# Kernel optimization log

Measured on AMD Instinct MI355X. Metric: run time of the kernel, lower is better.

The kernel has to match this reference:

```python
import jax, jax.numpy as jnp
import numpy as np
from jax.scipy.special import logsumexp

TAG_NAMES = ['<pad>', 'O', 'B-PER', 'I-PER', 'B-LOC', 'I-LOC', 'B-ORG', 'I-ORG', 'B-MISC', 'I-MISC']
K = len(TAG_NAMES)
T, B, D = 512, 64, 1024
PAD = 0
IMP = -100.0
VOCAB = 30000


def _crf_params(rng):
    # torchcrf reset_parameters: uniform(-0.1, 0.1), then init_crf_transitions overrides
    start = rng.uniform(-0.1, 0.1, K).astype(np.float32)
    end = rng.uniform(-0.1, 0.1, K).astype(np.float32)
    trans = rng.uniform(-0.1, 0.1, (K, K)).astype(np.float32)
    for i, name in enumerate(TAG_NAMES):
        if name[0] in ('I', 'L') or name == '<pad>':
            start[i] = IMP
        if name[0] in ('B', 'I'):
            end[i] = IMP
    tag_is = {p: [i for i, t in enumerate(TAG_NAMES) if t[0] == p] for p in 'BIOUL'}
    tag_is['P'] = [i for i, t in enumerate(TAG_NAMES) if t == 'tag']
    for ft, tos in {'B': 'BOUP', 'I': 'BOUP', 'O': 'IL', 'U': 'IL'}.items():
        for fi in tag_is[ft]:
            for tt in tos:
                for ti in tag_is[tt]:
                    trans[fi, ti] = IMP
    for ft, tos in {'B': 'IL', 'I': 'IL'}.items():
        for fi in tag_is[ft]:
            for tt in tos:
                for ti in tag_is[tt]:
                    if TAG_NAMES[fi].split('-')[1] != TAG_NAMES[ti].split('-')[1]:
                        trans[fi, ti] = IMP
    return jnp.asarray(start), jnp.asarray(end), jnp.asarray(trans)


def setup_inputs() -> dict:
    rng = np.random.default_rng(0)
    # torchcrf requires mask[0] == 1 everywhere and contiguous masks -> build from lengths
    lengths = rng.integers(T // 2, T + 1, size=B)
    valid = np.arange(T)[:, None] < lengths[None, :]  # (T, B)
    words = np.where(valid, rng.integers(1, VOCAB, size=(T, B)), PAD).astype(np.int64)
    tags = rng.integers(0, K, size=(T, B)).astype(np.int64)
    word_features = rng.standard_normal((T, B, D)).astype(np.float32)
    W = (rng.standard_normal((D, K)) / np.sqrt(D)).astype(np.float32)
    b = np.zeros(K, np.float32)
    start, end, trans = _crf_params(rng)
    return dict(words=jnp.asarray(words), tags=jnp.asarray(tags),
                word_features=jnp.asarray(word_features), W=jnp.asarray(W), b=jnp.asarray(b),
                start_trans=start, end_trans=end, transitions=trans)


def _crf_loss(emissions, tags, maskf, start, end, trans):
    """-log p(tags | emissions), summed over batch (torchcrf reduction='sum')."""
    bidx = jnp.arange(emissions.shape[1])
    # gold-path score (numerator)
    score0 = start[tags[0]] + emissions[0, bidx, tags[0]]
    em_tag = jnp.take_along_axis(emissions[1:], tags[1:, :, None], axis=-1)[..., 0]  # (T-1,B)
    step = trans[tags[:-1], tags[1:]] + em_tag
    numer = score0 + jnp.sum(step * maskf[1:], axis=0)
    seq_ends = maskf.sum(0).astype(jnp.int32) - 1
    numer = numer + end[tags[seq_ends, bidx]]
    # partition function (forward algorithm, stable log-sum-exp scan)
    def fwd_step(score, xs):
        em_t, m_t = xs
        nxt = logsumexp(score[:, :, None] + trans[None] + em_t[:, None, :], axis=1)  # (B,K)
        return jnp.where(m_t[:, None] > 0, nxt, score), None
    score, _ = jax.lax.scan(fwd_step, start[None] + emissions[0], (emissions[1:], maskf[1:]))
    denom = logsumexp(score + end[None], axis=1)
    return -(numer - denom).sum()


def _crf_decode(emissions, maskf, start, end, trans):
    """Viterbi decode; returns (T,B) int32 paths, 0-padded past sequence ends."""
    bidx = jnp.arange(emissions.shape[1])
    def vit_step(score, xs):
        em_t, m_t = xs
        bcast = score[:, :, None] + trans[None] + em_t[:, None, :]  # (B, K_prev, K_cur)
        best = bcast.max(axis=1)
        idx = bcast.argmax(axis=1).astype(jnp.int32)
        return jnp.where(m_t[:, None] > 0, best, score), idx
    score, history = jax.lax.scan(vit_step, start[None] + emissions[0], (emissions[1:], maskf[1:]))
    last_tag = jnp.argmax(score + end[None], axis=1).astype(jnp.int32)  # tag at seq_end per batch
    def back_step(tag, xs):
        hist_t, m_t = xs
        prev = jnp.where(m_t > 0, hist_t[bidx, tag], tag)
        return prev, prev
    _, path_head = jax.lax.scan(back_step, last_tag, (history, maskf[1:]), reverse=True)
    paths = jnp.concatenate([path_head, last_tag[None]], axis=0)  # (T, B)
    return jnp.where(maskf > 0, paths, 0)


def reference(words, tags, word_features, W, b, start_trans, end_trans, transitions):
    # eval-mode dropout is identity; fc projects features to tag emissions
    emissions = word_features @ W + b  # (T, B, K)
    maskf = (words != PAD).astype(emissions.dtype)  # (T, B)
    paths = _crf_decode(emissions, maskf, start_trans, end_trans, transitions)
    loss = _crf_loss(emissions, tags, maskf, start_trans, end_trans, transitions)
    return paths, loss
```

## Files before the change

kernel.cpp:

```cpp
#include <hip/hip_runtime.h>
#include <hip/hip_bf16.h>

#define TT 512
#define BB 64
#define KK 10
#define DD 1024
#define CL 32
#define NC 16

typedef unsigned char uchar;
typedef short bf16x8 __attribute__((ext_vector_type(8)));
typedef float f32x4 __attribute__((ext_vector_type(4)));

__device__ __forceinline__ unsigned f2bf(float f) {
    unsigned u = __float_as_uint(f);
    return (u + 0x7FFFu + ((u >> 16) & 1u)) >> 16;
}

__device__ __forceinline__ float max10(const float* r) {
    float m0 = fmaxf(r[0], r[1]), m1 = fmaxf(r[2], r[3]);
    float m2 = fmaxf(r[4], r[5]), m3 = fmaxf(r[6], r[7]);
    float m4 = fmaxf(r[8], r[9]);
    m0 = fmaxf(m0, m1); m2 = fmaxf(m2, m3); m0 = fmaxf(m0, m2);
    return fmaxf(m0, m4);
}

__device__ __forceinline__ float lse10(const float* r) {
    const float m = max10(r);
    float s0 = __expf(r[0] - m) + __expf(r[1] - m);
    float s1 = __expf(r[2] - m) + __expf(r[3] - m);
    float s2 = __expf(r[4] - m) + __expf(r[5] - m);
    float s3 = __expf(r[6] - m) + __expf(r[7] - m);
    float s4 = __expf(r[8] - m) + __expf(r[9] - m);
    return m + __logf(((s0 + s1) + (s2 + s3)) + s4);
}

__global__ __launch_bounds__(512) void k_emissions(
    const int* __restrict__ words, const float* __restrict__ wf,
    const float* __restrict__ W, const float* __restrict__ bias,
    float* __restrict__ em, int* __restrict__ lenArr, float* loss_slot) {
    __shared__ char  Ab[2][128 * 256];
    __shared__ uint4 Bfrag[32][64];
    __shared__ int   cnt[8][64];

    const int tid = threadIdx.x;

    for (int idx = tid; idx < 32 * 64; idx += 512) {
        const int ks = idx >> 6, l = idx & 63;
        const int col = l & 15, kg = l >> 4;
        unsigned u[4];
        #pragma unroll
        for (int p = 0; p < 4; ++p) {
            unsigned lo = 0, hi = 0;
            if (col < KK) {
                const int k0 = ks * 32 + kg * 8 + p * 2;
                lo = f2bf(W[(size_t)k0 * KK + col]);
                hi = f2bf(W[(size_t)(k0 + 1) * KK + col]);
            }
            u[p] = lo | (hi << 16);
        }
        Bfrag[ks][l] = make_uint4(u[0], u[1], u[2], u[3]);
    }

    const int wave = tid >> 6, lane = tid & 63;
    const int arow = lane & 15;
    const int kg   = lane >> 4;
    const int row0blk = blockIdx.x * 128;

    const int srow = tid >> 5;
    const int scol = (tid & 31) * 4;
    const float* gbase = wf + (size_t)(row0blk + srow) * DD + scol;
    const int wr_off = srow * 256 + (((scol >> 3) ^ srow) << 4) + ((scol & 7) * 2);

    float4 st[8];
    #pragma unroll
    for (int i = 0; i < 8; ++i) st[i] = *(const float4*)(gbase + i * 16384);
    #pragma unroll
    for (int i = 0; i < 8; ++i) {
        uint2 w;
        w.x = (__float_as_uint(st[i].x) >> 16) | (__float_as_uint(st[i].y) & 0xFFFF0000u);
        w.y = (__float_as_uint(st[i].z) >> 16) | (__float_as_uint(st[i].w) & 0xFFFF0000u);
        *(uint2*)(&Ab[0][wr_off + i * 4096]) = w;
    }
    #pragma unroll
    for (int i = 0; i < 8; ++i) st[i] = *(const float4*)(gbase + 128 + i * 16384);
    __syncthreads();

    f32x4 acc = {0.f, 0.f, 0.f, 0.f};
    const int ldsrow = wave * 16 + arow;

    #pragma unroll 1
    for (int p = 0; p < 8; ++p) {
        if (p < 7) {
            if (p > 0) __syncthreads();
            char* wb = Ab[(p + 1) & 1];
            #pragma unroll
            for (int i = 0; i < 8; ++i) {
                uint2 w;
                w.x = (__float_as_uint(st[i].x) >> 16) | (__float_as_uint(st[i].y) & 0xFFFF0000u);
                w.y = (__float_as_uint(st[i].z) >> 16) | (__float_as_uint(st[i].w) & 0xFFFF0000u);
                *(uint2*)(&wb[wr_off + i * 4096]) = w;
            }
            if (p < 6) {
                const float* gp = gbase + (size_t)(p + 2) * 128;
                #pragma unroll
                for (int i = 0; i < 8; ++i) st[i] = *(const float4*)(gp + i * 16384);
            }
            __syncthreads();
        }
        const char* rb = &Ab[p & 1][ldsrow * 256];
        #pragma unroll
        for (int ks = 0; ks < 4; ++ks) {
            const bf16x8 a = *(const bf16x8*)(rb + (((ks * 4 + kg) ^ arow) << 4));
            union { uint4 u; bf16x8 v; } bu;
            bu.u = Bfrag[p * 4 + ks][lane];
            acc = __builtin_amdgcn_mfma_f32_16x16x32_bf16(a, bu.v, acc, 0, 0, 0);
        }
    }

    const int row0 = row0blk + wave * 16;
    if (arow < KK) {
        const float bk = bias[arow];
        #pragma unroll
        for (int r = 0; r < 4; ++r)
            em[(size_t)(row0 + kg * 4 + r) * KK + arow] = acc[r] + bk;
    }

    if (blockIdx.x == 0) {
        const int b = tid & 63, seg = tid >> 6;
        int c = 0;
        for (int t = seg; t < TT; t += 8) c += (words[t * BB + b] != 0) ? 1 : 0;
        cnt[seg][b] = c;
        __syncthreads();
        if (tid < 64) {
            int s = 0;
            #pragma unroll
            for (int g = 0; g < 8; ++g) s += cnt[g][tid];
            lenArr[tid] = s;
        }
        if (tid == 0) *loss_slot = 0.f;
    }
}

__global__ __launch_bounds__(128) void k_chunk(
    const float* __restrict__ em, const float* __restrict__ trans,
    const int* __restrict__ lenArr, float* __restrict__ Mlse, float* __restrict__ Mmax) {
    int id = blockIdx.x;
    const bool mx = id >= 1024; id &= 1023;
    const int b = id >> 4, c = id & 15;
    const int len = lenArr[b];
    const int s_lo = c * CL + 1;
    const int s_hi = min(c * CL + CL, len - 1);
    const int ns = s_hi - s_lo + 1;
    if (ns <= 0) return;

    __shared__ float Ms[KK][12];
    __shared__ float eml[CL][KK];
    const int tid = threadIdx.x;
    for (int idx = tid; idx < CL * KK; idx += 128) {
        const int sl = idx / KK, j = idx % KK;
        const int s = s_lo + sl;
        eml[sl][j] = (s <= TT - 1) ? em[((size_t)s * BB + b) * KK + j] : 0.f;
    }
    const int i = tid / KK, j = tid % KK;
    const bool act = tid < KK * KK;
    float trc[KK];
    if (act) {
        #pragma unroll
        for (int k = 0; k < KK; ++k) trc[k] = trans[k * KK + j];
    }
    __syncthreads();
    float cur = 0.f;
    if (act) { cur = trans[i * KK + j] + eml[0][j]; Ms[i][j] = cur; }
    __syncthreads();
    for (int sl = 1; sl < ns; ++sl) {
        float row[KK];
        if (act) {
            #pragma unroll
            for (int k = 0; k < KK; ++k) row[k] = Ms[i][k] + trc[k];
        }
        __syncthreads();
        if (act) {
            cur = (mx ? max10(row) : lse10(row)) + eml[sl][j];
            Ms[i][j] = cur;
        }
        __syncthreads();
    }
    if (act) {
        float* out = mx ? Mmax : Mlse;
        out[((size_t)b * NC + c) * 100 + i * KK + j] = cur;
    }
}

__global__ __launch_bounds__(1024) void k_crf(
    const int* __restrict__ tags, const float* __restrict__ em,
    const float* __restrict__ startv, const float* __restrict__ endv,
    const float* __restrict__ trans, const int* __restrict__ lenArr,
    const float* __restrict__ Mlse, const float* __restrict__ Mmax,
    int* __restrict__ paths, float* __restrict__ loss_slot) {
    const int b = blockIdx.x;
    const int tid = threadIdx.x;
    const int wv = tid >> 6, lane = tid & 63;
    const int len = lenArr[b];

    __shared__ float Ml[NC][100];
    __shared__ float Mm[NC][100];
    __shared__ float eml[NC][CL][KK];
    __shared__ float ub[NC][KK];
    __shared__ uchar hl[NC][CL * KK];
    __shared__ int   Fl[NC][KK];
    __shared__ int   vt[NC + 1];
    __shared__ float em0[KK];
    __shared__ float red[2];

    for (int idx = tid; idx < NC * 100; idx += 1024) {
        Ml[idx / 100][idx % 100] = Mlse[(size_t)b * NC * 100 + idx];
        Mm[idx / 100][idx % 100] = Mmax[(size_t)b * NC * 100 + idx];
    }
    for (int idx = tid; idx < NC * CL * KK; idx += 1024) {
        const int c = idx / (CL * KK), r = idx % (CL * KK);
        const int sl = r / KK, j = r % KK;
        const int s = c * CL + 1 + sl;
        eml[c][sl][j] = (s <= TT - 1) ? em[((size_t)s * BB + b) * KK + j] : 0.f;
    }
    if (tid < KK) em0[tid] = em[(size_t)b * KK + tid];
    __syncthreads();

    if (wv == 0) {
        float v[KK];
        #pragma unroll
        for (int i = 0; i < KK; ++i) v[i] = startv[i] + em0[i];
        for (int c = 0; c < NC; ++c) {
            if (lane < KK) ub[c][lane] = v[lane];
            const int s_hi = min(c * CL + CL, len - 1);
            if (s_hi >= c * CL + 1) {
                float nv = 0.f;
                if (lane < KK) {
                    float r[KK];
                    #pragma unroll
                    for (int k = 0; k < KK; ++k) r[k] = v[k] + Mm[c][k * KK + lane];
                    nv = max10(r);
                }
                #pragma unroll
                for (int i = 0; i < KK; ++i) v[i] = __shfl(nv, i);
            }
        }
        float best = v[0] + endv[0];
        int bi = 0;
        #pragma unroll
        for (int i = 1; i < KK; ++i) {
            const float x = v[i] + endv[i];
            if (x > best) { best = x; bi = i; }
        }
        if (lane == 0) vt[NC] = bi;
    } else if (wv == 1) {
        float v[KK];
        #pragma unroll
        for (int i = 0; i < KK; ++i) v[i] = startv[i] + em0[i];
        for (int c = 0; c < NC; ++c) {
            const int s_hi = min(c * CL + CL, len - 1);
            if (s_hi >= c * CL + 1) {
                float nv = 0.f;
                if (lane < KK) {
                    float r[KK];
                    #pragma unroll
                    for (int k = 0; k < KK; ++k) r[k] = v[k] + Ml[c][k * KK + lane];
                    nv = lse10(r);
                }
                #pragma unroll
                for (int i = 0; i < KK; ++i) v[i] = __shfl(nv, i);
            }
        }
        float r[KK];
        #pragma unroll
        for (int i = 0; i < KK; ++i) r[i] = v[i] + endv[i];
        if (lane == 0) red[0] = lse10(r);
    } else if (wv == 2) {
        float part = 0.f;
        for (int t = 1 + lane; t < len; t += 64) {
            const int tp = tags[(t - 1) * BB + b];
            const int tc = tags[t * BB + b];
            part += trans[tp * KK + tc] + eml[(t - 1) >> 5][(t - 1) & 31][tc];
        }
        #pragma unroll
        for (int off = 32; off >= 1; off >>= 1) part += __shfl_xor(part, off);
        if (lane == 0) {
            const int t0 = tags[b];
            const int te = tags[(len - 1) * BB + b];
            red[1] = part + startv[t0] + em0[t0] + endv[te];
        }
    }
    __syncthreads();

    {
        const int c = wv;
        const int s_hi = min(c * CL + CL, len - 1);
        const int ns = s_hi - (c * CL + 1) + 1;
        if (ns > 0) {
            float trc[KK];
            if (lane < KK) {
                #pragma unroll
                for (int i = 0; i < KK; ++i) trc[i] = trans[i * KK + lane];
            }
            float s[KK];
            #pragma unroll
            for (int i = 0; i < KK; ++i) s[i] = ub[c][i];
            for (int sl = 0; sl < ns; ++sl) {
                float best = s[0] + trc[0];
                int bi = 0;
                #pragma unroll
                for (int i = 1; i < KK; ++i) {
                    const float x = s[i] + trc[i];
                    if (x > best) { best = x; bi = i; }
                }
                float snew = 0.f;
                if (lane < KK) {
                    snew = best + eml[c][sl][lane];
                    hl[c][sl * KK + lane] = (uchar)bi;
                }
                #pragma unroll
                for (int i = 0; i < KK; ++i) s[i] = __shfl(snew, i);
            }
            if (lane < KK) {
                int cur = lane;
                for (int sl = ns - 1; sl >= 0; --sl) cur = hl[c][sl * KK + cur];
                Fl[c][lane] = cur;
            }
        }
    }
    __syncthreads();

    if (tid == 0) {
        int cur = vt[NC];
        for (int c = NC - 1; c >= 0; --c) {
            const int s_hi = min(c * CL + CL, len - 1);
            if (s_hi >= c * CL + 1) cur = Fl[c][cur];
            vt[c] = cur;
        }
        atomicAdd(loss_slot, red[0] - red[1]);
    }
    __syncthreads();

    const int t0 = wv * CL;
    if (lane < CL) {
        const int t = t0 + lane;
        if (t >= len) paths[t * BB + b] = 0;
    }
    if (lane == 0) {
        const int a = min(t0 + CL, len - 1);
        if (a >= t0) {
            int cur = vt[wv + 1];
            for (int t = a; t >= t0; --t) {
                if (t <= t0 + CL - 1) paths[t * BB + b] = cur;
                if (t > t0) cur = (int)hl[wv][(t - t0 - 1) * KK + cur];
            }
        }
    }
}

extern "C" void kernel_launch(void* const* d_in, const int* in_sizes, int n_in,
                              void* d_out, int out_size, void* d_ws, size_t ws_size,
                              hipStream_t stream) {
    const int*   words  = (const int*)d_in[0];
    const int*   tags   = (const int*)d_in[1];
    const float* wf     = (const float*)d_in[2];
    const float* W      = (const float*)d_in[3];
    const float* bias   = (const float*)d_in[4];
    const float* startv = (const float*)d_in[5];
    const float* endv   = (const float*)d_in[6];
    const float* trans  = (const float*)d_in[7];

    float* em   = (float*)d_ws;
    float* Mlse = em + 327680;
    float* Mmax = Mlse + 102400;
    int*   lenA = (int*)(Mmax + 102400);

    int*   paths     = (int*)d_out;
    float* loss_slot = ((float*)d_out) + TT * BB;

    k_emissions<<<256, 512, 0, stream>>>(words, wf, W, bias, em, lenA, loss_slot);
    k_chunk<<<2048, 128, 0, stream>>>(em, trans, lenA, Mlse, Mmax);
    k_crf<<<64, 1024, 0, stream>>>(tags, em, startv, endv, trans, lenA,
                                   Mlse, Mmax, paths, loss_slot);
}
```

Baseline: 82.75 us.

## Double-buffer emission prefetch registers and halve barriers in the GEMM loop

The emission GEMM k-loop is rewritten as a fully unrolled ping-pong over two register slots, stA and stB, so global prefetch runs two chunks ahead. Each phase loads its LDS A/B fragments first, issues the next global loads, then runs the MFMAs and writes the converted bf16 tile into the other LDS buffer. This replaces the two __syncthreads per iteration with a single raw s_barrier after an lgkmcnt wait. Feature loads now use nontemporal hints, which avoids polluting cache with the 128 MB streaming input. The cost is higher register pressure from the two 8-wide float4 slots, and correctness depends on the hand-placed barrier ordering.

After: 84.47 us. +2.1%, slower.

```diff
diff --git a/kernel.cpp b/kernel.cpp
--- a/kernel.cpp
+++ b/kernel.cpp
@@ -47,13 +47,13 @@
 
     for (int idx = tid; idx < 32 * 64; idx += 512) {
         const int ks = idx >> 6, l = idx & 63;
-        const int col = l & 15, kg = l >> 4;
+        const int col = l & 15, kg2 = l >> 4;
         unsigned u[4];
         #pragma unroll
         for (int p = 0; p < 4; ++p) {
             unsigned lo = 0, hi = 0;
             if (col < KK) {
-                const int k0 = ks * 32 + kg * 8 + p * 2;
+                const int k0 = ks * 32 + kg2 * 8 + p * 2;
                 lo = f2bf(W[(size_t)k0 * KK + col]);
                 hi = f2bf(W[(size_t)(k0 + 1) * KK + col]);
             }
@@ -72,50 +72,64 @@
     const float* gbase = wf + (size_t)(row0blk + srow) * DD + scol;
     const int wr_off = srow * 256 + (((scol >> 3) ^ srow) << 4) + ((scol & 7) * 2);
 
-    float4 st[8];
+#define CVT_WRITE(SLOT, BUFIDX) do { \
+    char* wb_ = &Ab[BUFIDX][0]; \
+    _Pragma("unroll") \
+    for (int i_ = 0; i_ < 8; ++i_) { \
+        uint2 w_; \
+        w_.x = (__float_as_uint(SLOT[i_][0]) >> 16) | (__float_as_uint(SLOT[i_][1]) & 0xFFFF0000u); \
+        w_.y = (__float_as_uint(SLOT[i_][2]) >> 16) | (__float_as_uint(SLOT[i_][3]) & 0xFFFF0000u); \
+        *(uint2*)(&wb_[wr_off + i_ * 4096]) = w_; \
+    } \
+} while (0)
+
+    f32x4 stA[8], stB[8];
     #pragma unroll
-    for (int i = 0; i < 8; ++i) st[i] = *(const float4*)(gbase + i * 16384);
+    for (int i = 0; i < 8; ++i)
+        stA[i] = __builtin_nontemporal_load((const f32x4*)(gbase + i * 16384));
     #pragma unroll
-    for (int i = 0; i < 8; ++i) {
-        uint2 w;
-        w.x = (__float_as_uint(st[i].x) >> 16) | (__float_as_uint(st[i].y) & 0xFFFF0000u);
-        w.y = (__float_as_uint(st[i].z) >> 16) | (__float_as_uint(st[i].w) & 0xFFFF0000u);
-        *(uint2*)(&Ab[0][wr_off + i * 4096]) = w;
-    }
-    #pragma unroll
-    for (int i = 0; i < 8; ++i) st[i] = *(const float4*)(gbase + 128 + i * 16384);
-    __syncthreads();
+    for (int i = 0; i < 8; ++i)
+        stB[i] = __builtin_nontemporal_load((const f32x4*)(gbase + 128 + i * 16384));
+    CVT_WRITE(stA, 0);
+    asm volatile("s_waitcnt lgkmcnt(0)" ::: "memory");
+    __builtin_amdgcn_s_barrier();
+    __builtin_amdgcn_sched_barrier(0);
 
     f32x4 acc = {0.f, 0.f, 0.f, 0.f};
     const int ldsrow = wave * 16 + arow;
 
-    #pragma unroll 1
-    for (int p = 0; p < 8; ++p) {
-        if (p < 7) {
-            if (p > 0) __syncthreads();
-            char* wb = Ab[(p + 1) & 1];
-            #pragma unroll
-            for (int i = 0; i < 8; ++i) {
-                uint2 w;
-                w.x = (__float_as_uint(st[i].x) >> 16) | (__float_as_uint(st[i].y) & 0xFFFF0000u);
-                w.y = (__float_as_uint(st[i].z) >> 16) | (__float_as_uint(st[i].w) & 0xFFFF0000u);
-                *(uint2*)(&wb[wr_off + i * 4096]) = w;
-            }
-            if (p < 6) {
-                const float* gp = gbase + (size_t)(p + 2) * 128;
-                #pragma unroll
-                for (int i = 0; i < 8; ++i) st[i] = *(const float4*)(gp + i * 16384);
-            }
-            __syncthreads();
-        }
-        const char* rb = &Ab[p & 1][ldsrow * 256];
-        #pragma unroll
-        for (int ks = 0; ks < 4; ++ks) {
-            const bf16x8 a = *(const bf16x8*)(rb + (((ks * 4 + kg) ^ arow) << 4));
-            union { uint4 u; bf16x8 v; } bu;
-            bu.u = Bfrag[p * 4 + ks][lane];
-            acc = __builtin_amdgcn_mfma_f32_16x16x32_bf16(a, bu.v, acc, 0, 0, 0);
-        }
+#define PHASE(PIDX, RDBUF, PRESLOT, WRSLOT, WRBUF, DO_PRE, DO_WR) do { \
+    bf16x8 a_[4]; uint4 bf_[4]; \
+    const char* rb_ = &Ab[RDBUF][ldsrow * 256]; \
+    _Pragma("unroll") \
+    for (int ks_ = 0; ks_ < 4; ++ks_) { \
+        a_[ks_] = *(const bf16x8*)(rb_ + ((((ks_ * 4) + kg) ^ arow) << 4)); \
+        bf_[ks_] = Bfrag[(PIDX) * 4 + ks_][lane]; \
+    } \
+    if (DO_PRE) { \
+        const float* gp_ = gbase + (size_t)((PIDX) + 2) * 128; \
+        _Pragma("unroll") \
+        for (int i_ = 0; i_ < 8; ++i_) \
+            PRESLOT[i_] = __builtin_nontemporal_load((const f32x4*)(gp_ + i_ * 16384)); \
+    } \
+    _Pragma("unroll") \
+    for (int ks_ = 0; ks_ < 4; ++ks_) { \
+        union { uint4 u; bf16x8 v; } bu_; bu_.u = bf_[ks_]; \
+        acc = __builtin_amdgcn_mfma_f32_16x16x32_bf16(a_[ks_], bu_.v, acc, 0, 0, 0); \
+    } \
+    if (DO_WR) { \
+        CVT_WRITE(WRSLOT, WRBUF); \
+        asm volatile("s_waitcnt lgkmcnt(0)" ::: "memory"); \
+        __builtin_amdgcn_s_barrier(); \
+        __builtin_amdgcn_sched_barrier(0); \
+    } \
+} while (0)
+
+    #pragma unroll
+    for (int pp = 0; pp < 4; ++pp) {
+        const int p0 = pp * 2;
+        PHASE(p0,     0, stA, stB, 1, (pp < 3), true);
+        PHASE(p0 + 1, 1, stB, stA, 0, (pp < 3), (pp < 3));
     }
 
     const int row0 = row0blk + wave * 16;
@@ -140,6 +154,8 @@
         }
         if (tid == 0) *loss_slot = 0.f;
     }
+#undef PHASE
+#undef CVT_WRITE
 }
 
 __global__ __launch_bounds__(128) void k_chunk(
```
